# Performance work log

Hardware: AMD Instinct MI355X
Metric: run time of the kernel (lower is better)

The kernel has to match this reference:

```python
import jax, jax.numpy as jnp
import numpy as np

B, STREAM, IN_CH = 128, 512, 4
EXTRA, GROUPS, DEPTH = 5, 2, 3
STEP, LENGTH = 16, 32
RNN, OUT = 256, 10
C = IN_CH + 1 + EXTRA              # augmented channels: original + time + 1x1-conv
SIG_C = C + C * C + C ** 3          # signature channels per group at depth 3
W = (STREAM - LENGTH) // STEP + 1   # number of sliding windows = GRU steps
F = GROUPS * SIG_C                  # GRU input features


def _outer(a, b):
    # flattened tensor (outer) product on last axis: (...,m),(...,n)->(...,m*n)
    return (a[..., :, None] * b[..., None, :]).reshape(a.shape[:-1] + (a.shape[-1] * b.shape[-1],))


def _chen_step(S, dx):
    # Chen's identity: S <- S (tensor) exp(dx). S is a tuple of flattened
    # signature levels (..., C^k), k=1..DEPTH; dx has shape (..., C).
    P = [jnp.ones(dx.shape[:-1] + (1,), dx.dtype)]  # dx^{(x)j}/j!, j=0..DEPTH
    for j in range(1, DEPTH + 1):
        P.append(_outer(P[-1], dx) / j)
    newS = []
    for k in range(1, DEPTH + 1):
        acc = P[k]  # S_0 (x) P_k
        for j in range(k):
            acc = acc + _outer(S[k - 1 - j], P[j])
        newS.append(acc)
    return tuple(newS)


def setup_inputs() -> dict:
    key = jax.random.key(0)
    ks = jax.random.split(key, 10)
    s_aug = 1.0 / np.sqrt(IN_CH)
    s_rnn = 1.0 / np.sqrt(RNN)
    return {
        "x": jax.random.normal(ks[0], (B, STREAM, IN_CH), jnp.float32),
        "W_aug": jax.random.uniform(ks[1], (GROUPS, EXTRA, IN_CH), jnp.float32, -s_aug, s_aug),
        "b_aug": jax.random.uniform(ks[2], (GROUPS, EXTRA), jnp.float32, -s_aug, s_aug),
        "W_ih": jax.random.uniform(ks[3], (3 * RNN, F), jnp.float32, -s_rnn, s_rnn),
        "W_hh": jax.random.uniform(ks[4], (3 * RNN, RNN), jnp.float32, -s_rnn, s_rnn),
        "b_ih": jax.random.uniform(ks[5], (3 * RNN,), jnp.float32, -s_rnn, s_rnn),
        "b_hh": jax.random.uniform(ks[6], (3 * RNN,), jnp.float32, -s_rnn, s_rnn),
        "W_out": jax.random.uniform(ks[7], (OUT, RNN), jnp.float32, -s_rnn, s_rnn),
        "b_out": jax.random.uniform(ks[8], (OUT,), jnp.float32, -s_rnn, s_rnn),
    }


def reference(x, W_aug, b_aug, W_ih, W_hh, b_ih, b_hh, W_out, b_out):
    # (a) linear augmentation per channel group: [original | time | conv1x1(x)]
    t = jnp.linspace(0.0, 1.0, STREAM, dtype=x.dtype)
    t = jnp.broadcast_to(t[None, :, None], (B, STREAM, 1))
    aug = jnp.einsum('bsi,gei->bgse', x, W_aug) + b_aug[None, :, None, :]  # (B,G,S,EXTRA)
    base = jnp.broadcast_to(jnp.concatenate([x, t], -1)[:, None],
                            (B, GROUPS, STREAM, IN_CH + 1))
    xa = jnp.concatenate([base, aug], -1)            # (B,G,S,C)
    xa = xa.reshape(B * GROUPS, STREAM, C)

    # (b) depth-3 signatures over sliding windows via Chen's identity
    dx = xa[:, 1:] - xa[:, :-1]                       # (BG, S-1, C)
    widx = jnp.arange(W)[:, None] * STEP + jnp.arange(LENGTH - 1)[None, :]
    dxw = dx[:, widx]                                 # (BG, W, L-1, C)
    dxw = jnp.moveaxis(dxw, 2, 0)                     # (L-1, BG, W, C)
    S0 = tuple(jnp.zeros((B * GROUPS, W, C ** k), x.dtype) for k in range(1, DEPTH + 1))
    S, _ = jax.lax.scan(lambda S, d: (_chen_step(S, d), None), S0, dxw)
    sig = jnp.concatenate(S, -1)                      # (BG, W, SIG_C)
    sig = sig.reshape(B, GROUPS, W, SIG_C)
    sig = jnp.moveaxis(sig, 2, 0).reshape(W, B, F)    # (W, B, G*SIG_C)

    # (c) GRU over window signatures (torch.nn.GRUCell math, gate order r,z,n)
    def gru(h, xt):
        gi = xt @ W_ih.T + b_ih
        gh = h @ W_hh.T + b_hh
        ir, iz, inn = jnp.split(gi, 3, -1)
        hr, hz, hn = jnp.split(gh, 3, -1)
        r = jax.nn.sigmoid(ir + hr)
        z = jax.nn.sigmoid(iz + hz)
        n = jnp.tanh(inn + r * hn)
        return (1 - z) * n + z * h, None

    h, _ = jax.lax.scan(gru, jnp.zeros((B, RNN), x.dtype), sig)
    return jax.nn.sigmoid(h @ W_out.T + b_out)        # (B, OUT)
```

## Files before the change

kernel.cpp:

```cpp
#include <hip/hip_runtime.h>
#include <hip/hip_bf16.h>
#include <stdint.h>


typedef _Float16 f16;
typedef f16  f16x4 __attribute__((ext_vector_type(4)));
typedef f16  f16x8 __attribute__((ext_vector_type(8)));
typedef float f32x2 __attribute__((ext_vector_type(2)));
typedef float f32x4 __attribute__((ext_vector_type(4)));

#define ASYNC16(gp, lp) __builtin_amdgcn_global_load_lds( \
    (const __attribute__((address_space(1))) void*)(gp),  \
    (__attribute__((address_space(3))) void*)(lp), 16, 0, 0)

#define BAR_LDS() do { asm volatile("s_waitcnt lgkmcnt(0)" ::: "memory"); \
                       __builtin_amdgcn_s_barrier();                      \
                       asm volatile("" ::: "memory"); } while (0)

__device__ __forceinline__ float fexp2(float x) {
    float r; asm("v_exp_f32 %0, %1" : "=v"(r) : "v"(x)); return r;
}
__device__ __forceinline__ float frcp(float x) {
    float r; asm("v_rcp_f32 %0, %1" : "=v"(r) : "v"(x)); return r;
}

__global__ __launch_bounds__(256) void prep_kernel(const float* __restrict__ x,
                                                   const float* __restrict__ W_aug,
                                                   const float* __restrict__ Wih,
                                                   const float* __restrict__ Whh,
                                                   f16* __restrict__ sig16,
                                                   f16* __restrict__ wih16,
                                                   f16* __restrict__ whh16,
                                                   uint8_t* __restrict__ whh8) {
    __shared__ float dxs[4][31][10];
    const int tid = threadIdx.x;
    if (blockIdx.x < 840) {
        int c = blockIdx.x * 256 + tid;
        int r = c / 280, kc = (c - r * 280) * 8;
        const float* src = Wih + (size_t)r * 2220 + kc;
        f16x8 o;
        if (kc + 8 <= 2220) {
            float4 v0 = *(const float4*)(src);
            float4 v1 = *(const float4*)(src + 4);
            o[0]=(f16)v0.x; o[1]=(f16)v0.y; o[2]=(f16)v0.z; o[3]=(f16)v0.w;
            o[4]=(f16)v1.x; o[5]=(f16)v1.y; o[6]=(f16)v1.z; o[7]=(f16)v1.w;
        } else {
#pragma unroll
            for (int j = 0; j < 8; j++)
                o[j] = (f16)((kc + j < 2220) ? src[j] : 0.0f);
        }
        *(f16x8*)(wih16 + (size_t)r * 2240 + kc) = o;
        return;
    }
    if (blockIdx.x < 936) {
        int c2 = ((int)blockIdx.x - 840) * 256 + tid;
        int j8 = c2 * 8;
        float w[8];
        {
            float4 v0 = *(const float4*)(Whh + j8);
            float4 v1 = *(const float4*)(Whh + j8 + 4);
            w[0]=v0.x; w[1]=v0.y; w[2]=v0.z; w[3]=v0.w;
            w[4]=v1.x; w[5]=v1.y; w[6]=v1.z; w[7]=v1.w;
        }
        f16x8 o;
#pragma unroll
        for (int j = 0; j < 8; j++) o[j] = (f16)w[j];
        *(f16x8*)(whh16 + j8) = o;
        if (j8 < 131072) {
            uint32_t p01 = (uint32_t)__builtin_amdgcn_cvt_pk_fp8_f32(w[0]*16.f, w[1]*16.f, 0, false) & 0xffffu;
            uint32_t p23 = (uint32_t)__builtin_amdgcn_cvt_pk_fp8_f32(w[2]*16.f, w[3]*16.f, 0, false) & 0xffffu;
            uint32_t p45 = (uint32_t)__builtin_amdgcn_cvt_pk_fp8_f32(w[4]*16.f, w[5]*16.f, 0, false) & 0xffffu;
            uint32_t p67 = (uint32_t)__builtin_amdgcn_cvt_pk_fp8_f32(w[6]*16.f, w[7]*16.f, 0, false) & 0xffffu;
            uint2 st = make_uint2(p01 | (p23 << 16), p45 | (p67 << 16));
            *(uint2*)(whh8 + j8) = st;
        }
        return;
    }
    const int sub = tid >> 6, t64 = tid & 63;
    const int cid = ((int)blockIdx.x - 936) * 4 + sub;
    const int w = cid % 31;
    const int bg = cid / 31;
    const int b = bg >> 1, g = bg & 1;
    if (t64 < 31) {
        int s = w * 16 + t64;
        const float4 x0 = *(const float4*)(x + ((size_t)b * 512 + s) * 4);
        const float4 x1 = *(const float4*)(x + ((size_t)b * 512 + s + 1) * 4);
        float d0 = x1.x - x0.x, d1 = x1.y - x0.y, d2 = x1.z - x0.z, d3 = x1.w - x0.w;
        dxs[sub][t64][0] = d0; dxs[sub][t64][1] = d1;
        dxs[sub][t64][2] = d2; dxs[sub][t64][3] = d3;
        dxs[sub][t64][4] = 1.0f / 511.0f;
#pragma unroll
        for (int e = 0; e < 5; e++) {
            const float* wa = W_aug + (g * 5 + e) * 4;
            dxs[sub][t64][5 + e] = d0 * wa[0] + d1 * wa[1] + d2 * wa[2] + d3 * wa[3];
        }
    }
    __syncthreads();
    size_t base = ((size_t)(w * 128 + b)) * 2240 + (size_t)g * 1110;
    if (t64 < 50) {
        int p0 = 2 * t64, p1 = p0 + 1;
        int i0 = p0 / 10, j0 = p0 % 10, j1 = j0 + 1;
        const float* dz  = &dxs[sub][0][0];
        const float* pI  = dz + i0;
        const float* pJ0 = dz + j0;
        const float* pJ1 = dz + j1;
        float s3a[10], s3b[10];
#pragma unroll
        for (int k = 0; k < 10; k++) { s3a[k] = 0.f; s3b[k] = 0.f; }
        float s2a = 0.f, s2b = 0.f, s1 = 0.f;
        for (int l = 0; l < 31; l++) {
            const float* row = dz + l * 10;
            float di  = pI[l * 10];
            float dj0 = pJ0[l * 10];
            float dj1 = pJ1[l * 10];
            float t0 = s1 + di * (1.0f / 3.0f);
            float a0 = s2a + t0 * (0.5f * dj0);
            float a1 = s2b + t0 * (0.5f * dj1);
#pragma unroll
            for (int k = 0; k < 10; k++) {
                float dk = row[k];
                s3a[k] += a0 * dk;
                s3b[k] += a1 * dk;
            }
            float u = s1 + 0.5f * di;
            s2a += u * dj0;
            s2b += u * dj1;
            s1 += di;
        }
        sig16[base + 10 + p0] = (f16)s2a;
        sig16[base + 10 + p1] = (f16)s2b;
#pragma unroll
        for (int k = 0; k < 10; k++) {
            sig16[base + 110 + p0 * 10 + k] = (f16)s3a[k];
            sig16[base + 110 + p1 * 10 + k] = (f16)s3b[k];
        }
    } else if (t64 < 60) {
        int c = t64 - 50;
        const float* pc = &dxs[sub][0][0] + c;
        float s = 0.f;
        for (int l = 0; l < 31; l++) s += pc[l * 10];
        sig16[base + c] = (f16)s;
    }
    if (g == 1 && t64 < 20)
        sig16[((size_t)(w * 128 + b)) * 2240 + 2220 + t64] = (f16)0.0f;
}

__global__ __launch_bounds__(256) void gemm_kernel(const f16* __restrict__ A,
                                                   const f16* __restrict__ Bw,
                                                   const float* __restrict__ bias,
                                                   const float* __restrict__ bhh,
                                                   f16* __restrict__ Cgi) {
    const int lin = blockIdx.x;
    const int t = (lin & 7) + 8 * (lin / 48);
    const int nb = (lin >> 3) % 6;
    if (t >= 31) return;
    __shared__ __align__(16) f16 As[3][128 * 32];
    __shared__ __align__(16) f16 Bs[3][128 * 32];
    const int tid = threadIdx.x, lane = tid & 63, wid = tid >> 6;
    const int wm = wid >> 1, wn = wid & 1;
    const int Mbase = t * 128, Nbase = nb * 128;
    const int lr = lane >> 2, lk = lane & 3;
    const int l16 = lane & 15, quad = lane >> 4;
    const int r0a = wid * 32, r0b = wid * 32 + 16;
    const f16* gaA0 = A  + (size_t)(Mbase + r0a + lr) * 2240 + lk * 8;
    const f16* gaA1 = A  + (size_t)(Mbase + r0b + lr) * 2240 + lk * 8;
    const f16* gbB0 = Bw + (size_t)(Nbase + r0a + lr) * 2240 + lk * 8;
    const f16* gbB1 = Bw + (size_t)(Nbase + r0b + lr) * 2240 + lk * 8;

#define GISSUE(KT, BUF) do { \
        int _k0 = (KT) * 32; \
        ASYNC16(gaA0 + _k0, &As[BUF][r0a * 32]); \
        ASYNC16(gbB0 + _k0, &Bs[BUF][r0a * 32]); \
        ASYNC16(gaA1 + _k0, &As[BUF][r0b * 32]); \
        ASYNC16(gbB1 + _k0, &Bs[BUF][r0b * 32]); } while (0)

#define GCOMPUTE(BUF) do { \
        f16x8 af[4], bf[4]; \
        _Pragma("unroll") \
        for (int mt = 0; mt < 4; mt++) \
            af[mt] = *(const f16x8*)&As[BUF][(wm * 64 + mt * 16 + l16) * 32 + quad * 8]; \
        _Pragma("unroll") \
        for (int nt = 0; nt < 4; nt++) \
            bf[nt] = *(const f16x8*)&Bs[BUF][(wn * 64 + nt * 16 + l16) * 32 + quad * 8]; \
        _Pragma("unroll") \
        for (int mt = 0; mt < 4; mt++) \
            _Pragma("unroll") \
            for (int nt = 0; nt < 4; nt++) \
                acc[mt][nt] = __builtin_amdgcn_mfma_f32_16x16x32_f16(af[mt], bf[nt], acc[mt][nt], 0, 0, 0); } while (0)

    f32x4 acc[4][4];
#pragma unroll
    for (int mt = 0; mt < 4; mt++)
#pragma unroll
        for (int nt = 0; nt < 4; nt++) acc[mt][nt] = (f32x4){0.f, 0.f, 0.f, 0.f};

    GISSUE(0, 0);
    GISSUE(1, 1);
    for (int kt = 0; kt < 69; kt++) {
        asm volatile("s_waitcnt vmcnt(4) lgkmcnt(0)\n\ts_barrier" ::: "memory");
        if (kt < 68) GISSUE(kt + 2, (kt + 2) % 3);
        GCOMPUTE(kt % 3);
    }
    asm volatile("s_waitcnt vmcnt(0) lgkmcnt(0)\n\ts_barrier" ::: "memory");
    GCOMPUTE(0);

    const float NEG_LOG2E = -1.4426950408889634f;
    const float TWO_LOG2E =  2.8853900817779268f;
#pragma unroll
    for (int mt = 0; mt < 4; mt++) {
        const int bbv = wm * 4 + mt;
#pragma unroll
        for (int nt = 0; nt < 4; nt++) {
            int col = Nbase + wn * 64 + nt * 16 + l16;
            float bvv = bias[col] + (col < 512 ? bhh[col] : 0.0f);
            float scl = (col < 512) ? NEG_LOG2E : TWO_LOG2E;
            int gs = col >> 8, hcc = col & 255;
            int gw = hcc >> 5, gtc = (hcc >> 4) & 1, gl = hcc & 15;
            int u = gs * 2 + gtc;
            int gtid = gw * 64 + quad * 16 + gl;
            size_t off = ((size_t)((t * 8 + bbv) * 6 + u)) * 2048 + (size_t)gtid * 4;
            f16x4 st;
#pragma unroll
            for (int rr = 0; rr < 4; rr++) st[rr] = (f16)((acc[mt][nt][rr] + bvv) * scl);
            *(f16x4*)(Cgi + off) = st;
        }
    }
#undef GISSUE
#undef GCOMPUTE
}

#define ACLOB \
  "a0","a1","a2","a3","a4","a5","a6","a7","a8","a9","a10","a11","a12","a13","a14","a15", \
  "a16","a17","a18","a19","a20","a21","a22","a23","a24","a25","a26","a27","a28","a29","a30","a31", \
  "a32","a33","a34","a35","a36","a37","a38","a39","a40","a41","a42","a43","a44","a45","a46","a47", \
  "a48","a49","a50","a51","a52","a53","a54","a55","a56","a57","a58","a59","a60","a61","a62","a63", \
  "a64","a65","a66","a67","a68","a69","a70","a71","a72","a73","a74","a75","a76","a77","a78","a79", \
  "a80","a81","a82","a83","a84","a85","a86","a87","a88","a89","a90","a91","a92","a93","a94","a95", \
  "a96","a97","a98","a99","a100","a101","a102","a103","a104","a105","a106","a107","a108","a109","a110","a111", \
  "a112","a113","a114","a115","a116","a117","a118","a119","a120","a121","a122","a123","a124","a125","a126","a127", \
  "a128","a129","a130","a131","a132","a133","a134","a135","a136","a137","a138","a139","a140","a141","a142","a143", \
  "a144","a145","a146","a147","a148","a149","a150","a151","a152","a153","a154","a155"

#define LF8(A0,A1, U, KT) do { \
  f32x2 _t = *(const f32x2*)(whh8 + (size_t)(((U) >> 1) * 256 + wid * 32 + ((U) & 1) * 16 + l16) * 256 + (KT) * 32 + quad * 8); \
  asm volatile("v_accvgpr_write_b32 a" #A0 ", %0\n\t" \
               "v_accvgpr_write_b32 a" #A1 ", %1" \
               :: "v"(_t[0]), "v"(_t[1]) : "a" #A0, "a" #A1); } while (0)

#define LFN(A0,A1,A2,A3, TC, KT) do { \
  f32x4 _t = *(const f32x4*)(whh16 + (size_t)(512 + wid * 32 + (TC) * 16 + l16) * 256 + (KT) * 32 + quad * 8); \
  asm volatile("v_accvgpr_write_b32 a" #A0 ", %0\n\t" \
               "v_accvgpr_write_b32 a" #A1 ", %1\n\t" \
               "v_accvgpr_write_b32 a" #A2 ", %2\n\t" \
               "v_accvgpr_write_b32 a" #A3 ", %3" \
               :: "v"(_t[0]), "v"(_t[1]), "v"(_t[2]), "v"(_t[3]) \
               : "a" #A0, "a" #A1, "a" #A2, "a" #A3); } while (0)

#define FP8G(P, F0,F1,F2,F3) \
  "v_mfma_f32_16x16x32_fp8_fp8 a[128:131], " P ", a[" F0 "], a[128:131]\n\t" \
  "v_mfma_f32_16x16x32_fp8_fp8 a[132:135], " P ", a[" F1 "], a[132:135]\n\t" \
  "v_mfma_f32_16x16x32_fp8_fp8 a[136:139], " P ", a[" F2 "], a[136:139]\n\t" \
  "v_mfma_f32_16x16x32_fp8_fp8 a[140:143], " P ", a[" F3 "], a[140:143]\n\t"

#define FP8GZ(P, F0,F1,F2,F3) \
  "v_mfma_f32_16x16x32_fp8_fp8 a[128:131], " P ", a[" F0 "], a[152:155]\n\t" \
  "v_mfma_f32_16x16x32_fp8_fp8 a[132:135], " P ", a[" F1 "], a[152:155]\n\t" \
  "v_mfma_f32_16x16x32_fp8_fp8 a[136:139], " P ", a[" F2 "], a[152:155]\n\t" \
  "v_mfma_f32_16x16x32_fp8_fp8 a[140:143], " P ", a[" F3 "], a[152:155]\n\t"

#define F16G(Q, G0,G1) \
  "v_mfma_f32_16x16x32_f16 a[144:147], " Q ", a[" G0 "], a[144:147]\n\t" \
  "v_mfma_f32_16x16x32_f16 a[148:151], " Q ", a[" G1 "], a[148:151]\n\t"

#define F16GZ(Q, G0,G1) \
  "v_mfma_f32_16x16x32_f16 a[144:147], " Q ", a[" G0 "], a[152:155]\n\t" \
  "v_mfma_f32_16x16x32_f16 a[148:151], " Q ", a[" G1 "], a[152:155]\n\t"

__global__ __launch_bounds__(512, 2) void gru_kernel(const f16* __restrict__ gi,
                                                     const f16* __restrict__ whh16,
                                                     const uint8_t* __restrict__ whh8,
                                                     const float* __restrict__ b_hh,
                                                     const float* __restrict__ W_out,
                                                     const float* __restrict__ b_out,
                                                     float* __restrict__ out) {
    __shared__ __align__(16) f16 hbufF[2][16 * 280];
    __shared__ __align__(16) uint8_t hbuf8[2][16 * 272];
    const int tid = threadIdx.x, lane = tid & 63, wid = tid >> 6;
    const int quad = lane >> 4, l16 = lane & 15;
    const int bb = blockIdx.x;

    for (int i = tid; i < 16 * 280; i += 512) hbufF[1][i] = (f16)0.0f;
    for (int i = tid; i < 16 * 272; i += 512) hbuf8[1][i] = 0;

    LF8(0,1, 0,0);   LF8(2,3, 0,1);   LF8(4,5, 0,2);   LF8(6,7, 0,3);
    LF8(8,9, 0,4);   LF8(10,11, 0,5); LF8(12,13, 0,6); LF8(14,15, 0,7);
    LF8(16,17, 1,0); LF8(18,19, 1,1); LF8(20,21, 1,2); LF8(22,23, 1,3);
    LF8(24,25, 1,4); LF8(26,27, 1,5); LF8(28,29, 1,6); LF8(30,31, 1,7);
    LF8(32,33, 2,0); LF8(34,35, 2,1); LF8(36,37, 2,2); LF8(38,39, 2,3);
    LF8(40,41, 2,4); LF8(42,43, 2,5); LF8(44,45, 2,6); LF8(46,47, 2,7);
    LF8(48,49, 3,0); LF8(50,51, 3,1); LF8(52,53, 3,2); LF8(54,55, 3,3);
    LF8(56,57, 3,4); LF8(58,59, 3,5); LF8(60,61, 3,6); LF8(62,63, 3,7);
    LFN(64,65,66,67,   0,0); LFN(68,69,70,71,   0,1); LFN(72,73,74,75,   0,2); LFN(76,77,78,79,   0,3);
    LFN(80,81,82,83,   0,4); LFN(84,85,86,87,   0,5); LFN(88,89,90,91,   0,6); LFN(92,93,94,95,   0,7);
    LFN(96,97,98,99,   1,0); LFN(100,101,102,103, 1,1); LFN(104,105,106,107, 1,2); LFN(108,109,110,111, 1,3);
    LFN(112,113,114,115, 1,4); LFN(116,117,118,119, 1,5); LFN(120,121,122,123, 1,6); LFN(124,125,126,127, 1,7);
    {
        const float z = 0.0f;
        asm volatile("v_accvgpr_write_b32 a152, %0\n\t"
                     "v_accvgpr_write_b32 a153, %0\n\t"
                     "v_accvgpr_write_b32 a154, %0\n\t"
                     "v_accvgpr_write_b32 a155, %0"
                     :: "v"(z) : "a152","a153","a154","a155");
    }

    const float C2 = 2.8853900817779268f;
    float bhn[2];
#pragma unroll
    for (int tc = 0; tc < 2; tc++) bhn[tc] = C2 * b_hh[512 + wid * 32 + tc * 16 + l16];
    float hm[2][4];
#pragma unroll
    for (int tc = 0; tc < 2; tc++)
#pragma unroll
        for (int rr = 0; rr < 4; rr++) hm[tc][rr] = 0.f;

    uint32_t aF0 = (uint32_t)(uintptr_t)(__attribute__((address_space(3))) const void*)
                       (&hbufF[0][l16 * 280 + quad * 8]);
    uint32_t aF1 = (uint32_t)(uintptr_t)(__attribute__((address_space(3))) const void*)
                       (&hbufF[1][l16 * 280 + quad * 8]);
    uint32_t a80 = (uint32_t)(uintptr_t)(__attribute__((address_space(3))) const void*)
                       (&hbuf8[0][l16 * 272 + quad * 8]);
    uint32_t a81 = (uint32_t)(uintptr_t)(__attribute__((address_space(3))) const void*)
                       (&hbuf8[1][l16 * 272 + quad * 8]);

    const size_t lanebase = (size_t)bb * 12288 + (size_t)tid * 4;
    f16x4 gcur[6];
#pragma unroll
    for (int u = 0; u < 6; u++)
        gcur[u] = *(const f16x4*)(gi + lanebase + u * 2048);

    BAR_LDS();

    for (int t = 0; t < 31; t++) {
        const uint32_t a8 = (t & 1) ? a80 : a81;
        const uint32_t aF = (t & 1) ? aF0 : aF1;
        float cc[24];
        f32x2 p0, p1, p2;
        f32x4 q0, q1, q2;
        asm volatile(
            "ds_read_b64  %[p0], %[a8] offset:0\n\t"
            "ds_read_b128 %[q0], %[aF] offset:0\n\t"
            "ds_read_b64  %[p1], %[a8] offset:32\n\t"
            "ds_read_b128 %[q1], %[aF] offset:64\n\t"
            "ds_read_b64  %[p2], %[a8] offset:64\n\t"
            "ds_read_b128 %[q2], %[aF] offset:128\n\t"
            "s_waitcnt lgkmcnt(5)\n\t"
            FP8GZ("%[p0]", "0:1","16:17","32:33","48:49")
            "ds_read_b64  %[p0], %[a8] offset:96\n\t"
            "s_waitcnt lgkmcnt(5)\n\t"
            F16GZ("%[q0]", "64:67","96:99")
            "ds_read_b128 %[q0], %[aF] offset:192\n\t"
            "s_waitcnt lgkmcnt(5)\n\t"
            FP8G("%[p1]", "2:3","18:19","34:35","50:51")
            "ds_read_b64  %[p1], %[a8] offset:128\n\t"
            "s_waitcnt lgkmcnt(5)\n\t"
            F16G("%[q1]", "68:71","100:103")
            "ds_read_b128 %[q1], %[aF] offset:256\n\t"
            "s_waitcnt lgkmcnt(5)\n\t"
            FP8G("%[p2]", "4:5","20:21","36:37","52:53")
            "ds_read_b64  %[p2], %[a8] offset:160\n\t"
            "s_waitcnt lgkmcnt(5)\n\t"
            F16G("%[q2]", "72:75","104:107")
            "ds_read_b128 %[q2], %[aF] offset:320\n\t"
            "s_waitcnt lgkmcnt(5)\n\t"
            FP8G("%[p0]", "6:7","22:23","38:39","54:55")
            "ds_read_b64  %[p0], %[a8] offset:192\n\t"
            "s_waitcnt lgkmcnt(5)\n\t"
            F16G("%[q0]", "76:79","108:111")
            "ds_read_b128 %[q0], %[aF] offset:384\n\t"
            "s_waitcnt lgkmcnt(5)\n\t"
            FP8G("%[p1]", "8:9","24:25","40:41","56:57")
            "ds_read_b64  %[p1], %[a8] offset:224\n\t"
            "s_waitcnt lgkmcnt(5)\n\t"
            F16G("%[q1]", "80:83","112:115")
            "ds_read_b128 %[q1], %[aF] offset:448\n\t"
            "s_waitcnt lgkmcnt(5)\n\t"
            FP8G("%[p2]", "10:11","26:27","42:43","58:59")
            "s_waitcnt lgkmcnt(4)\n\t"
            F16G("%[q2]", "84:87","116:119")
            "s_waitcnt lgkmcnt(3)\n\t"
            FP8G("%[p0]", "12:13","28:29","44:45","60:61")
            "s_waitcnt lgkmcnt(2)\n\t"
            F16G("%[q0]", "88:91","120:123")
            "s_waitcnt lgkmcnt(1)\n\t"
            FP8G("%[p1]", "14:15","30:31","46:47","62:63")
            "s_waitcnt lgkmcnt(0)\n\t"
            F16G("%[q1]", "92:95","124:127")
            "s_nop 7\n\ts_nop 7\n\ts_nop 7\n\ts_nop 7\n\t"
            "v_accvgpr_read_b32 %[c0], a128\n\tv_accvgpr_read_b32 %[c1], a129\n\t"
            "v_accvgpr_read_b32 %[c2], a130\n\tv_accvgpr_read_b32 %[c3], a131\n\t"
            "v_accvgpr_read_b32 %[c4], a132\n\tv_accvgpr_read_b32 %[c5], a133\n\t"
            "v_accvgpr_read_b32 %[c6], a134\n\tv_accvgpr_read_b32 %[c7], a135\n\t"
            "v_accvgpr_read_b32 %[c8], a136\n\tv_accvgpr_read_b32 %[c9], a137\n\t"
            "v_accvgpr_read_b32 %[c10], a138\n\tv_accvgpr_read_b32 %[c11], a139\n\t"
            "v_accvgpr_read_b32 %[c12], a140\n\tv_accvgpr_read_b32 %[c13], a141\n\t"
            "v_accvgpr_read_b32 %[c14], a142\n\tv_accvgpr_read_b32 %[c15], a143\n\t"
            "v_accvgpr_read_b32 %[c16], a144\n\tv_accvgpr_read_b32 %[c17], a145\n\t"
            "v_accvgpr_read_b32 %[c18], a146\n\tv_accvgpr_read_b32 %[c19], a147\n\t"
            "v_accvgpr_read_b32 %[c20], a148\n\tv_accvgpr_read_b32 %[c21], a149\n\t"
            "v_accvgpr_read_b32 %[c22], a150\n\tv_accvgpr_read_b32 %[c23], a151"
            : [c0]"=v"(cc[0]), [c1]"=v"(cc[1]), [c2]"=v"(cc[2]), [c3]"=v"(cc[3]),
              [c4]"=v"(cc[4]), [c5]"=v"(cc[5]), [c6]"=v"(cc[6]), [c7]"=v"(cc[7]),
              [c8]"=v"(cc[8]), [c9]"=v"(cc[9]), [c10]"=v"(cc[10]), [c11]"=v"(cc[11]),
              [c12]"=v"(cc[12]), [c13]"=v"(cc[13]), [c14]"=v"(cc[14]), [c15]"=v"(cc[15]),
              [c16]"=v"(cc[16]), [c17]"=v"(cc[17]), [c18]"=v"(cc[18]), [c19]"=v"(cc[19]),
              [c20]"=v"(cc[20]), [c21]"=v"(cc[21]), [c22]"=v"(cc[22]), [c23]"=v"(cc[23]),
              [p0]"=&v"(p0), [p1]"=&v"(p1), [p2]"=&v"(p2),
              [q0]"=&v"(q0), [q1]"=&v"(q1), [q2]"=&v"(q2)
            : [a8]"v"(a8), [aF]"v"(aF)
            : ACLOB);

        f16* hdF = hbufF[t & 1];
        uint8_t* hd8 = hbuf8[t & 1];
        const float C1N16 = -0.09016844005556021f;
#pragma unroll
        for (int tc = 0; tc < 2; tc++) {
            const int hcx = wid * 32 + tc * 16 + l16;
#pragma unroll
            for (int rr = 0; rr < 4; rr++) {
                float rg = frcp(1.f + fexp2(fmaf(C1N16, cc[tc * 4 + rr],       (float)gcur[tc][rr])));
                float zg = frcp(1.f + fexp2(fmaf(C1N16, cc[(2 + tc) * 4 + rr], (float)gcur[2 + tc][rr])));
                float t2 = fmaf(rg, fmaf(C2, cc[16 + tc * 4 + rr], bhn[tc]), (float)gcur[4 + tc][rr]);
                float e2 = fexp2(t2);
                float ng = fmaf(-2.f, frcp(e2 + 1.f), 1.f);
                float h  = fmaf(zg, hm[tc][rr] - ng, ng);
                hm[tc][rr] = h;
                hdF[(quad * 4 + rr) * 280 + hcx] = (f16)h;
                int pk = __builtin_amdgcn_cvt_pk_fp8_f32(h, h, 0, false);
                hd8[(quad * 4 + rr) * 272 + hcx] = (uint8_t)pk;
            }
        }
        {
            int tn = (t < 30) ? t + 1 : 30;
            const f16* gsrc = gi + (size_t)tn * 98304 + lanebase;
#pragma unroll
            for (int u = 0; u < 6; u++)
                gcur[u] = *(const f16x4*)(gsrc + u * 2048);
        }
        BAR_LDS();
    }
    if (tid < 160) {
        int r = tid / 10, oc = tid - r * 10;
        const f16* hfin = hbufF[0];
        float s = b_out[oc];
        for (int k = 0; k < 256; k++) s += (float)hfin[r * 280 + k] * W_out[oc * 256 + k];
        out[(bb * 16 + r) * 10 + oc] = frcp(1.f + __expf(-s));
    }
}

extern "C" void kernel_launch(void* const* d_in, const int* in_sizes, int n_in,
                              void* d_out, int out_size, void* d_ws, size_t ws_size,
                              hipStream_t stream) {
    const float* x     = (const float*)d_in[0];
    const float* W_aug = (const float*)d_in[1];
    const float* W_ih  = (const float*)d_in[3];
    const float* W_hh  = (const float*)d_in[4];
    const float* b_ih  = (const float*)d_in[5];
    const float* b_hh  = (const float*)d_in[6];
    const float* W_out = (const float*)d_in[7];
    const float* b_out = (const float*)d_in[8];
    float* out = (float*)d_out;

    char* ws = (char*)d_ws;
    const size_t SIG_BYTES  = (size_t)3968 * 2240 * 2;
    const size_t WIH_BYTES  = (size_t)768 * 2240 * 2;
    const size_t WHH_BYTES  = (size_t)768 * 256 * 2;
    const size_t WHH8_BYTES = (size_t)512 * 256;
    const size_t GI_BYTES   = (size_t)31 * 8 * 6 * 512 * 4 * 2;
    if (ws_size < SIG_BYTES + WIH_BYTES + WHH_BYTES + WHH8_BYTES + GI_BYTES) return;
    f16* sig16    = (f16*)ws;
    f16* wih16    = (f16*)(ws + SIG_BYTES);
    f16* whh16    = (f16*)(ws + SIG_BYTES + WIH_BYTES);
    uint8_t* whh8 = (uint8_t*)(ws + SIG_BYTES + WIH_BYTES + WHH_BYTES);
    f16* giw      = (f16*)(ws + SIG_BYTES + WIH_BYTES + WHH_BYTES + WHH8_BYTES);

    hipLaunchKernelGGL(prep_kernel, dim3(2920), dim3(256), 0, stream,
                       x, W_aug, W_ih, W_hh, sig16, wih16, whh16, whh8);
    hipLaunchKernelGGL(gemm_kernel, dim3(192), dim3(256), 0, stream,
                       sig16, wih16, b_ih, b_hh, giw);
    hipLaunchKernelGGL(gru_kernel, dim3(8), dim3(512), 0, stream,
                       giw, whh16, whh8, b_hh, W_out, b_out, out);
}
```

Measured before the change: 213.5 us.

## Deepen GEMM LDS pipeline to seven stages and keep GRU accumulators in VGPRs

The input-projection GEMM now uses a seven-buffer LDS ring with six tiles in flight instead of three buffers with two in flight. The aim is to hide more global-load latency, at the cost of much more shared memory per block and likely lower occupancy. In the GRU step kernel, the MFMA accumulators are now register operands bound directly in VGPRs, which removes the 24 accvgpr reads and most of the s_nop padding. The step's MFMA phase is also wrapped in s_setprio 1 so that wave is scheduled ahead of others while it issues its matrix work.

```diff
diff --git a/kernel.cpp b/kernel.cpp
--- a/kernel.cpp
+++ b/kernel.cpp
@@ -154,8 +154,8 @@
     const int t = (lin & 7) + 8 * (lin / 48);
     const int nb = (lin >> 3) % 6;
     if (t >= 31) return;
-    __shared__ __align__(16) f16 As[3][128 * 32];
-    __shared__ __align__(16) f16 Bs[3][128 * 32];
+    __shared__ __align__(16) f16 As[7][128 * 32];
+    __shared__ __align__(16) f16 Bs[7][128 * 32];
     const int tid = threadIdx.x, lane = tid & 63, wid = tid >> 6;
     const int wm = wid >> 1, wn = wid & 1;
     const int Mbase = t * 128, Nbase = nb * 128;
@@ -194,15 +194,16 @@
 #pragma unroll
         for (int nt = 0; nt < 4; nt++) acc[mt][nt] = (f32x4){0.f, 0.f, 0.f, 0.f};
 
-    GISSUE(0, 0);
-    GISSUE(1, 1);
-    for (int kt = 0; kt < 69; kt++) {
-        asm volatile("s_waitcnt vmcnt(4) lgkmcnt(0)\n\ts_barrier" ::: "memory");
-        if (kt < 68) GISSUE(kt + 2, (kt + 2) % 3);
-        GCOMPUTE(kt % 3);
+    GISSUE(0, 0); GISSUE(1, 1); GISSUE(2, 2);
+    GISSUE(3, 3); GISSUE(4, 4); GISSUE(5, 5);
+    for (int kt = 0; kt < 64; kt++) {
+        asm volatile("s_waitcnt vmcnt(20) lgkmcnt(0)\n\ts_barrier" ::: "memory");
+        GISSUE(kt + 6, (kt + 6) % 7);
+        GCOMPUTE(kt % 7);
     }
     asm volatile("s_waitcnt vmcnt(0) lgkmcnt(0)\n\ts_barrier" ::: "memory");
-    GCOMPUTE(0);
+    GCOMPUTE(64 % 7); GCOMPUTE(65 % 7); GCOMPUTE(66 % 7);
+    GCOMPUTE(67 % 7); GCOMPUTE(68 % 7); GCOMPUTE(69 % 7);
 
     const float NEG_LOG2E = -1.4426950408889634f;
     const float TWO_LOG2E =  2.8853900817779268f;
@@ -237,9 +238,7 @@
   "a64","a65","a66","a67","a68","a69","a70","a71","a72","a73","a74","a75","a76","a77","a78","a79", \
   "a80","a81","a82","a83","a84","a85","a86","a87","a88","a89","a90","a91","a92","a93","a94","a95", \
   "a96","a97","a98","a99","a100","a101","a102","a103","a104","a105","a106","a107","a108","a109","a110","a111", \
-  "a112","a113","a114","a115","a116","a117","a118","a119","a120","a121","a122","a123","a124","a125","a126","a127", \
-  "a128","a129","a130","a131","a132","a133","a134","a135","a136","a137","a138","a139","a140","a141","a142","a143", \
-  "a144","a145","a146","a147","a148","a149","a150","a151","a152","a153","a154","a155"
+  "a112","a113","a114","a115","a116","a117","a118","a119","a120","a121","a122","a123","a124","a125","a126","a127"
 
 #define LF8(A0,A1, U, KT) do { \
   f32x2 _t = *(const f32x2*)(whh8 + (size_t)(((U) >> 1) * 256 + wid * 32 + ((U) & 1) * 16 + l16) * 256 + (KT) * 32 + quad * 8); \
@@ -256,25 +255,25 @@
                :: "v"(_t[0]), "v"(_t[1]), "v"(_t[2]), "v"(_t[3]) \
                : "a" #A0, "a" #A1, "a" #A2, "a" #A3); } while (0)
 
+#define FP8GZ(P, F0,F1,F2,F3) \
+  "v_mfma_f32_16x16x32_fp8_fp8 %[aR0], " P ", a[" F0 "], %[zq]\n\t" \
+  "v_mfma_f32_16x16x32_fp8_fp8 %[aR1], " P ", a[" F1 "], %[zq]\n\t" \
+  "v_mfma_f32_16x16x32_fp8_fp8 %[aZ0], " P ", a[" F2 "], %[zq]\n\t" \
+  "v_mfma_f32_16x16x32_fp8_fp8 %[aZ1], " P ", a[" F3 "], %[zq]\n\t"
+
 #define FP8G(P, F0,F1,F2,F3) \
-  "v_mfma_f32_16x16x32_fp8_fp8 a[128:131], " P ", a[" F0 "], a[128:131]\n\t" \
-  "v_mfma_f32_16x16x32_fp8_fp8 a[132:135], " P ", a[" F1 "], a[132:135]\n\t" \
-  "v_mfma_f32_16x16x32_fp8_fp8 a[136:139], " P ", a[" F2 "], a[136:139]\n\t" \
-  "v_mfma_f32_16x16x32_fp8_fp8 a[140:143], " P ", a[" F3 "], a[140:143]\n\t"
-
-#define FP8GZ(P, F0,F1,F2,F3) \
-  "v_mfma_f32_16x16x32_fp8_fp8 a[128:131], " P ", a[" F0 "], a[152:155]\n\t" \
-  "v_mfma_f32_16x16x32_fp8_fp8 a[132:135], " P ", a[" F1 "], a[152:155]\n\t" \
-  "v_mfma_f32_16x16x32_fp8_fp8 a[136:139], " P ", a[" F2 "], a[152:155]\n\t" \
-  "v_mfma_f32_16x16x32_fp8_fp8 a[140:143], " P ", a[" F3 "], a[152:155]\n\t"
+  "v_mfma_f32_16x16x32_fp8_fp8 %[aR0], " P ", a[" F0 "], %[aR0]\n\t" \
+  "v_mfma_f32_16x16x32_fp8_fp8 %[aR1], " P ", a[" F1 "], %[aR1]\n\t" \
+  "v_mfma_f32_16x16x32_fp8_fp8 %[aZ0], " P ", a[" F2 "], %[aZ0]\n\t" \
+  "v_mfma_f32_16x16x32_fp8_fp8 %[aZ1], " P ", a[" F3 "], %[aZ1]\n\t"
+
+#define F16GZ(Q, G0,G1) \
+  "v_mfma_f32_16x16x32_f16 %[aN0], " Q ", a[" G0 "], %[zq]\n\t" \
+  "v_mfma_f32_16x16x32_f16 %[aN1], " Q ", a[" G1 "], %[zq]\n\t"
 
 #define F16G(Q, G0,G1) \
-  "v_mfma_f32_16x16x32_f16 a[144:147], " Q ", a[" G0 "], a[144:147]\n\t" \
-  "v_mfma_f32_16x16x32_f16 a[148:151], " Q ", a[" G1 "], a[148:151]\n\t"
-
-#define F16GZ(Q, G0,G1) \
-  "v_mfma_f32_16x16x32_f16 a[144:147], " Q ", a[" G0 "], a[152:155]\n\t" \
-  "v_mfma_f32_16x16x32_f16 a[148:151], " Q ", a[" G1 "], a[152:155]\n\t"
+  "v_mfma_f32_16x16x32_f16 %[aN0], " Q ", a[" G0 "], %[aN0]\n\t" \
+  "v_mfma_f32_16x16x32_f16 %[aN1], " Q ", a[" G1 "], %[aN1]\n\t"
 
 __global__ __launch_bounds__(512, 2) void gru_kernel(const f16* __restrict__ gi,
                                                      const f16* __restrict__ whh16,
@@ -304,14 +303,6 @@
     LFN(80,81,82,83,   0,4); LFN(84,85,86,87,   0,5); LFN(88,89,90,91,   0,6); LFN(92,93,94,95,   0,7);
     LFN(96,97,98,99,   1,0); LFN(100,101,102,103, 1,1); LFN(104,105,106,107, 1,2); LFN(108,109,110,111, 1,3);
     LFN(112,113,114,115, 1,4); LFN(116,117,118,119, 1,5); LFN(120,121,122,123, 1,6); LFN(124,125,126,127, 1,7);
-    {
-        const float z = 0.0f;
-        asm volatile("v_accvgpr_write_b32 a152, %0\n\t"
-                     "v_accvgpr_write_b32 a153, %0\n\t"
-                     "v_accvgpr_write_b32 a154, %0\n\t"
-                     "v_accvgpr_write_b32 a155, %0"
-                     :: "v"(z) : "a152","a153","a154","a155");
-    }
 
     const float C2 = 2.8853900817779268f;
     float bhn[2];
@@ -338,15 +329,18 @@
     for (int u = 0; u < 6; u++)
         gcur[u] = *(const f16x4*)(gi + lanebase + u * 2048);
 
+    const f32x4 zq = (f32x4){0.f, 0.f, 0.f, 0.f};
+
     BAR_LDS();
 
     for (int t = 0; t < 31; t++) {
         const uint32_t a8 = (t & 1) ? a80 : a81;
         const uint32_t aF = (t & 1) ? aF0 : aF1;
-        float cc[24];
+        f32x4 aR0, aR1, aZ0, aZ1, aN0, aN1;
         f32x2 p0, p1, p2;
         f32x4 q0, q1, q2;
         asm volatile(
+            "s_setprio 1\n\t"
             "ds_read_b64  %[p0], %[a8] offset:0\n\t"
             "ds_read_b128 %[q0], %[aF] offset:0\n\t"
             "ds_read_b64  %[p1], %[a8] offset:32\n\t"
@@ -395,28 +389,13 @@
             FP8G("%[p1]", "14:15","30:31","46:47","62:63")
             "s_waitcnt lgkmcnt(0)\n\t"
             F16G("%[q1]", "92:95","124:127")
-            "s_nop 7\n\ts_nop 7\n\ts_nop 7\n\ts_nop 7\n\t"
-            "v_accvgpr_read_b32 %[c0], a128\n\tv_accvgpr_read_b32 %[c1], a129\n\t"
-            "v_accvgpr_read_b32 %[c2], a130\n\tv_accvgpr_read_b32 %[c3], a131\n\t"
-            "v_accvgpr_read_b32 %[c4], a132\n\tv_accvgpr_read_b32 %[c5], a133\n\t"
-            "v_accvgpr_read_b32 %[c6], a134\n\tv_accvgpr_read_b32 %[c7], a135\n\t"
-            "v_accvgpr_read_b32 %[c8], a136\n\tv_accvgpr_read_b32 %[c9], a137\n\t"
-            "v_accvgpr_read_b32 %[c10], a138\n\tv_accvgpr_read_b32 %[c11], a139\n\t"
-            "v_accvgpr_read_b32 %[c12], a140\n\tv_accvgpr_read_b32 %[c13], a141\n\t"
-            "v_accvgpr_read_b32 %[c14], a142\n\tv_accvgpr_read_b32 %[c15], a143\n\t"
-            "v_accvgpr_read_b32 %[c16], a144\n\tv_accvgpr_read_b32 %[c17], a145\n\t"
-            "v_accvgpr_read_b32 %[c18], a146\n\tv_accvgpr_read_b32 %[c19], a147\n\t"
-            "v_accvgpr_read_b32 %[c20], a148\n\tv_accvgpr_read_b32 %[c21], a149\n\t"
-            "v_accvgpr_read_b32 %[c22], a150\n\tv_accvgpr_read_b32 %[c23], a151"
-            : [c0]"=v"(cc[0]), [c1]"=v"(cc[1]), [c2]"=v"(cc[2]), [c3]"=v"(cc[3]),
-              [c4]"=v"(cc[4]), [c5]"=v"(cc[5]), [c6]"=v"(cc[6]), [c7]"=v"(cc[7]),
-              [c8]"=v"(cc[8]), [c9]"=v"(cc[9]), [c10]"=v"(cc[10]), [c11]"=v"(cc[11]),
-              [c12]"=v"(cc[12]), [c13]"=v"(cc[13]), [c14]"=v"(cc[14]), [c15]"=v"(cc[15]),
-              [c16]"=v"(cc[16]), [c17]"=v"(cc[17]), [c18]"=v"(cc[18]), [c19]"=v"(cc[19]),
-              [c20]"=v"(cc[20]), [c21]"=v"(cc[21]), [c22]"=v"(cc[22]), [c23]"=v"(cc[23]),
+            "s_setprio 0\n\t"
+            "s_nop 7\n\ts_nop 7"
+            : [aR0]"=&v"(aR0), [aR1]"=&v"(aR1), [aZ0]"=&v"(aZ0), [aZ1]"=&v"(aZ1),
+              [aN0]"=&v"(aN0), [aN1]"=&v"(aN1),
               [p0]"=&v"(p0), [p1]"=&v"(p1), [p2]"=&v"(p2),
               [q0]"=&v"(q0), [q1]"=&v"(q1), [q2]"=&v"(q2)
-            : [a8]"v"(a8), [aF]"v"(aF)
+            : [a8]"v"(a8), [aF]"v"(aF), [zq]"v"(zq)
             : ACLOB);
 
         f16* hdF = hbufF[t & 1];
@@ -425,11 +404,14 @@
 #pragma unroll
         for (int tc = 0; tc < 2; tc++) {
             const int hcx = wid * 32 + tc * 16 + l16;
+            const f32x4 vR = tc ? aR1 : aR0;
+            const f32x4 vZ = tc ? aZ1 : aZ0;
+            const f32x4 vN = tc ? aN1 : aN0;
 #pragma unroll
             for (int rr = 0; rr < 4; rr++) {
-                float rg = frcp(1.f + fexp2(fmaf(C1N16, cc[tc * 4 + rr],       (float)gcur[tc][rr])));
-                float zg = frcp(1.f + fexp2(fmaf(C1N16, cc[(2 + tc) * 4 + rr], (float)gcur[2 + tc][rr])));
-                float t2 = fmaf(rg, fmaf(C2, cc[16 + tc * 4 + rr], bhn[tc]), (float)gcur[4 + tc][rr]);
+                float rg = frcp(1.f + fexp2(fmaf(C1N16, vR[rr], (float)gcur[tc][rr])));
+                float zg = frcp(1.f + fexp2(fmaf(C1N16, vZ[rr], (float)gcur[2 + tc][rr])));
+                float t2 = fmaf(rg, fmaf(C2, vN[rr], bhn[tc]), (float)gcur[4 + tc][rr]);
                 float e2 = fexp2(t2);
                 float ng = fmaf(-2.f, frcp(e2 + 1.f), 1.f);
                 float h  = fmaf(zg, hm[tc][rr] - ng, ng);
```

New measurement: 212.4 us. No clear change (-0.5%).
